# Optimization experiments

Hardware: AMD Instinct MI355X
Metric: run time of the kernel (lower is better)

## Reference

```python
import jax, jax.numpy as jnp
import numpy as np

D_MODEL = 1024
D_STATE = 16
D_CONV = 4
EXPAND = 2
MLP_EXPAND = 2
D_INNER = EXPAND * D_MODEL          # 2048
DT_RANK = (D_MODEL + 15) // 16      # 64
BATCH, SEQ = 2, 1024


def setup_inputs() -> dict:
    key = jax.random.key(0)
    ks = jax.random.split(key, 16)
    s = 0.02
    inp = {
        "x": jax.random.normal(ks[0], (BATCH, SEQ, D_MODEL), jnp.float32),
        "norm1_g": jnp.ones((D_MODEL,), jnp.float32),
        "norm1_b": jnp.zeros((D_MODEL,), jnp.float32),
        "in_proj_w": jax.random.normal(ks[1], (2 * D_INNER, D_MODEL), jnp.float32) * s,
        "conv_w": jax.random.normal(ks[2], (D_INNER, 1, D_CONV), jnp.float32) * s,
        "conv_b": jnp.zeros((D_INNER,), jnp.float32),
        "x_proj_w": jax.random.normal(ks[3], (DT_RANK + 2 * D_STATE, D_INNER), jnp.float32) * s,
        "dt_proj_w": jax.random.normal(ks[4], (D_INNER, DT_RANK), jnp.float32) * s,
        "dt_proj_b": jax.random.normal(ks[5], (D_INNER,), jnp.float32) * 0.1,
        "A_log": jnp.log(jnp.broadcast_to(jnp.arange(1, D_STATE + 1, dtype=jnp.float32), (D_INNER, D_STATE))),
        "D_param": jnp.ones((D_INNER,), jnp.float32),
        "out_proj_w": jax.random.normal(ks[6], (D_MODEL, D_INNER), jnp.float32) * s,
        "norm2_g": jnp.ones((D_MODEL,), jnp.float32),
        "norm2_b": jnp.zeros((D_MODEL,), jnp.float32),
        "mlp_w1": jax.random.normal(ks[7], (MLP_EXPAND * D_MODEL, D_MODEL), jnp.float32) * s,
        "mlp_b1": jnp.zeros((MLP_EXPAND * D_MODEL,), jnp.float32),
        "mlp_w2": jax.random.normal(ks[8], (D_MODEL, MLP_EXPAND * D_MODEL), jnp.float32) * s,
        "mlp_b2": jnp.zeros((D_MODEL,), jnp.float32),
    }
    return inp


def _layernorm(x, g, b, eps=1e-5):
    m = jnp.mean(x, axis=-1, keepdims=True)
    v = jnp.var(x, axis=-1, keepdims=True)
    return (x - m) * jax.lax.rsqrt(v + eps) * g + b


def _silu(x):
    return x * jax.nn.sigmoid(x)


def _mamba(x, in_proj_w, conv_w, conv_b, x_proj_w, dt_proj_w, dt_proj_b, A_log, D_param, out_proj_w):
    # x: (B, L, d_model)
    xz = x @ in_proj_w.T                              # (B, L, 2*Di)
    xc, z = jnp.split(xz, 2, axis=-1)                 # each (B, L, Di)
    # causal depthwise conv over time
    xc_t = xc.transpose(0, 2, 1)                      # (B, Di, L)
    xc_t = jax.lax.conv_general_dilated(
        xc_t, conv_w, window_strides=(1,), padding=[(D_CONV - 1, 0)],
        dimension_numbers=("NCH", "OIH", "NCH"), feature_group_count=D_INNER,
    ) + conv_b[None, :, None]
    xc = _silu(xc_t).transpose(0, 2, 1)               # (B, L, Di)

    dbc = xc @ x_proj_w.T                             # (B, L, dt_rank + 2N)
    dt, Bm, Cm = jnp.split(dbc, [DT_RANK, DT_RANK + D_STATE], axis=-1)
    dt = jax.nn.softplus(dt @ dt_proj_w.T + dt_proj_b)  # (B, L, Di)
    A = -jnp.exp(A_log)                               # (Di, N)

    def step(h, inp):
        dt_t, B_t, C_t, x_t = inp                     # (B,Di),(B,N),(B,N),(B,Di)
        dA = jnp.exp(dt_t[..., None] * A)             # (B, Di, N)
        h = dA * h + (dt_t * x_t)[..., None] * B_t[:, None, :]
        y = jnp.einsum("bdn,bn->bd", h, C_t)
        return h, y

    h0 = jnp.zeros((x.shape[0], D_INNER, D_STATE), x.dtype)
    xs = (dt.transpose(1, 0, 2), Bm.transpose(1, 0, 2), Cm.transpose(1, 0, 2), xc.transpose(1, 0, 2))
    _, ys = jax.lax.scan(step, h0, xs)                # ys: (L, B, Di)
    y = ys.transpose(1, 0, 2) + xc * D_param          # skip term D*x
    y = y * _silu(z)
    return y @ out_proj_w.T                           # (B, L, d_model)


def reference(x, norm1_g, norm1_b, in_proj_w, conv_w, conv_b, x_proj_w, dt_proj_w,
              dt_proj_b, A_log, D_param, out_proj_w, norm2_g, norm2_b,
              mlp_w1, mlp_b1, mlp_w2, mlp_b2):
    # residual + Mamba(LN(x))  (droppath=0 -> identity)
    h = x + _mamba(_layernorm(x, norm1_g, norm1_b), in_proj_w, conv_w, conv_b,
                   x_proj_w, dt_proj_w, dt_proj_b, A_log, D_param, out_proj_w)
    # residual + MLP(LN(h))    (dropout eval -> identity)
    m = _layernorm(h, norm2_g, norm2_b)
    m = jax.nn.gelu(m @ mlp_w1.T + mlp_b1, approximate=False) @ mlp_w2.T + mlp_b2
    return h + m
```

## Files before the change

kernel.cpp:

```cpp
#include <hip/hip_runtime.h>
#include <math.h>

#define D_MODEL 1024
#define D_INNER 2048
#define DT_RANK 64
#define D_STATE 16
#define NBC 96
#define BATCH 2
#define SEQ 1024
#define TOK (BATCH*SEQ)
#define CS 32
#define NCH 32
#define XKSPLIT 16

typedef __attribute__((ext_vector_type(8))) short short8;
typedef __attribute__((ext_vector_type(4))) float f32x4;
typedef __attribute__((ext_vector_type(4))) unsigned short us4;

__device__ __forceinline__ float softplus_f(float x) {
    return (x > 20.0f) ? x : log1pf(__expf(x));
}
__device__ __forceinline__ float gelu_f(float x) {
    return 0.5f * x * (1.0f + erff(x * 0.70710678118654752f));
}
__device__ __forceinline__ float silu_f(float x) {
    return x / (1.0f + __expf(-x));
}
__device__ __forceinline__ ushort f2bf(float f) {
    unsigned u = __float_as_uint(f);
    unsigned r = (u + 0x7fffu + ((u >> 16) & 1u)) >> 16;
    return (ushort)r;
}
__device__ __forceinline__ float bf2f(ushort u) {
    return __uint_as_float(((unsigned)u) << 16);
}

__global__ void convert_weights_kernel(const float* __restrict__ Wp, const float* __restrict__ Wo,
                                       const float* __restrict__ W1, const float* __restrict__ W2,
                                       const float* __restrict__ Wx, const float* __restrict__ Wdt,
                                       ushort* __restrict__ Wpb, ushort* __restrict__ Wob,
                                       ushort* __restrict__ W1b, ushort* __restrict__ W2b,
                                       ushort* __restrict__ Wxb, ushort* __restrict__ Wdtb) {
    int i = blockIdx.x * 256 + threadIdx.x;
    const float* src; ushort* dst; int off;
    if      (i < 1048576) { src = Wp;  dst = Wpb;  off = i; }
    else if (i < 1572864) { src = Wo;  dst = Wob;  off = i - 1048576; }
    else if (i < 2097152) { src = W1;  dst = W1b;  off = i - 1572864; }
    else if (i < 2621440) { src = W2;  dst = W2b;  off = i - 2097152; }
    else if (i < 2670592) { src = Wx;  dst = Wxb;  off = i - 2621440; }
    else if (i < 2703360) { src = Wdt; dst = Wdtb; off = i - 2670592; }
    else return;
    float4 v = ((const float4*)src)[off];
    ushort4 o;
    o.x = f2bf(v.x); o.y = f2bf(v.y); o.z = f2bf(v.z); o.w = f2bf(v.w);
    ((ushort4*)dst)[off] = o;
}

__global__ void ln_bf16_kernel(const float* __restrict__ x, const float* __restrict__ g,
                               const float* __restrict__ b, ushort* __restrict__ out) {
    int row = blockIdx.x;
    const float* xr = x + (size_t)row * D_MODEL;
    ushort* outr = out + (size_t)row * D_MODEL;
    int tid = threadIdx.x;
    float4 v = ((const float4*)xr)[tid];
    float s  = v.x + v.y + v.z + v.w;
    float sq = v.x*v.x + v.y*v.y + v.z*v.z + v.w*v.w;
    #pragma unroll
    for (int o = 32; o > 0; o >>= 1) {
        s  += __shfl_down(s,  o);
        sq += __shfl_down(sq, o);
    }
    __shared__ float ss[4], ssq[4];
    int wid = tid >> 6, lane = tid & 63;
    if (lane == 0) { ss[wid] = s; ssq[wid] = sq; }
    __syncthreads();
    if (tid == 0) {
        float a = 0.f, c = 0.f;
        for (int i = 0; i < 4; i++) { a += ss[i]; c += ssq[i]; }
        ss[0] = a; ssq[0] = c;
    }
    __syncthreads();
    float mean = ss[0] * (1.0f / D_MODEL);
    float var  = ssq[0] * (1.0f / D_MODEL) - mean * mean;
    float rstd = rsqrtf(var + 1e-5f);
    float4 gg = ((const float4*)g)[tid];
    float4 bb = ((const float4*)b)[tid];
    ushort4 o;
    o.x = f2bf((v.x - mean) * rstd * gg.x + bb.x);
    o.y = f2bf((v.y - mean) * rstd * gg.y + bb.y);
    o.z = f2bf((v.z - mean) * rstd * gg.z + bb.z);
    o.w = f2bf((v.w - mean) * rstd * gg.w + bb.w);
    ((ushort4*)outr)[tid] = o;
}

template<int BM, int BN, int ACT, bool BIAS, bool RES, bool OUTBF>
__global__ __launch_bounds__(256)
void mfma_gemm(const ushort* __restrict__ A, const ushort* __restrict__ W,
               const float* __restrict__ bias,
               const float* __restrict__ res, int ldr,
               void* __restrict__ Cout, int ldc, int K) {
    constexpr int WM = BM / 2, WN = BN / 2, FM = WM / 16, FN = WN / 16;
    __shared__ __align__(16) ushort As[BM * 32];
    __shared__ __align__(16) ushort Ws[BN * 32];
    const int tid  = threadIdx.x;
    const int lane = tid & 63, w = tid >> 6;
    const int wr = w >> 1, wc = w & 1;
    const int row0 = blockIdx.y * BM, col0 = blockIdx.x * BN;
    const int l16 = lane >> 4, l15 = lane & 15;
    const int srow = tid >> 2;
    const int scol = (tid & 3) * 8;

    f32x4 acc[FM][FN] = {};

    for (int k0 = 0; k0 < K; k0 += 32) {
        #pragma unroll
        for (int s = 0; s < BM / 64; s++) {
            const ushort* g = A + (size_t)(row0 + s * 64 + srow) * K + k0 + scol;
            __builtin_amdgcn_global_load_lds(
                (const __attribute__((address_space(1))) void*)g,
                (__attribute__((address_space(3))) void*)((char*)As + s * 4096 + w * 1024),
                16, 0, 0);
        }
        #pragma unroll
        for (int s = 0; s < BN / 64; s++) {
            const ushort* g = W + (size_t)(col0 + s * 64 + srow) * K + k0 + scol;
            __builtin_amdgcn_global_load_lds(
                (const __attribute__((address_space(1))) void*)g,
                (__attribute__((address_space(3))) void*)((char*)Ws + s * 4096 + w * 1024),
                16, 0, 0);
        }
        __syncthreads();

        short8 a[FM], b[FN];
        #pragma unroll
        for (int m = 0; m < FM; m++)
            a[m] = *(const short8*)(As + (wr * WM + m * 16 + l15) * 32 + l16 * 8);
        #pragma unroll
        for (int n = 0; n < FN; n++)
            b[n] = *(const short8*)(Ws + (wc * WN + n * 16 + l15) * 32 + l16 * 8);
        #pragma unroll
        for (int m = 0; m < FM; m++)
            #pragma unroll
            for (int n = 0; n < FN; n++)
                acc[m][n] = __builtin_amdgcn_mfma_f32_16x16x32_bf16(a[m], b[n], acc[m][n], 0, 0, 0);
        __syncthreads();
    }

    #pragma unroll
    for (int m = 0; m < FM; m++) {
        const int r0 = row0 + wr * WM + m * 16 + l16 * 4;
        #pragma unroll
        for (int n = 0; n < FN; n++) {
            const int c = col0 + wc * WN + n * 16 + l15;
            const float bv = BIAS ? bias[c] : 0.f;
            #pragma unroll
            for (int q = 0; q < 4; q++) {
                const int r = r0 + q;
                float v = acc[m][n][q] + bv;
                if (ACT == 1) v = softplus_f(v);
                else if (ACT == 2) v = gelu_f(v);
                if (RES) v += res[(size_t)r * ldr + c];
                if (OUTBF) ((ushort*)Cout)[(size_t)r * ldc + c] = f2bf(v);
                else       ((float*)Cout)[(size_t)r * ldc + c] = v;
            }
        }
    }
}

__global__ __launch_bounds__(256)
void xproj_split_kernel(const ushort* __restrict__ A,
                        const ushort* __restrict__ W,
                        float* __restrict__ part) {
    __shared__ __align__(16) ushort As[128 * 64];
    __shared__ __align__(16) ushort Bs[96 * 64];
    const int tid = threadIdx.x;
    const int lane = tid & 63, w = tid >> 6;
    const int l16 = lane >> 4, l15 = lane & 15;
    const int kbase = blockIdx.x * (D_INNER / XKSPLIT);
    const int row0 = blockIdx.y * 128;
    const int srow = tid >> 3;
    const int scol = (tid & 7) * 8;

    f32x4 acc[2][6] = {};

    for (int k0 = 0; k0 < D_INNER / XKSPLIT; k0 += 64) {
        #pragma unroll
        for (int s = 0; s < 4; s++) {
            const ushort* g = A + (size_t)(row0 + s * 32 + srow) * D_INNER + kbase + k0 + scol;
            __builtin_amdgcn_global_load_lds(
                (const __attribute__((address_space(1))) void*)g,
                (__attribute__((address_space(3))) void*)((char*)As + s * 4096 + w * 1024),
                16, 0, 0);
        }
        #pragma unroll
        for (int s = 0; s < 3; s++) {
            const ushort* g = W + (size_t)(s * 32 + srow) * D_INNER + kbase + k0 + scol;
            __builtin_amdgcn_global_load_lds(
                (const __attribute__((address_space(1))) void*)g,
                (__attribute__((address_space(3))) void*)((char*)Bs + s * 4096 + w * 1024),
                16, 0, 0);
        }
        __syncthreads();
        #pragma unroll
        for (int ks = 0; ks < 2; ks++) {
            short8 a[2], b[6];
            #pragma unroll
            for (int m = 0; m < 2; m++)
                a[m] = *(const short8*)(As + (w * 32 + m * 16 + l15) * 64 + ks * 32 + l16 * 8);
            #pragma unroll
            for (int n = 0; n < 6; n++)
                b[n] = *(const short8*)(Bs + (n * 16 + l15) * 64 + ks * 32 + l16 * 8);
            #pragma unroll
            for (int m = 0; m < 2; m++)
                #pragma unroll
                for (int n = 0; n < 6; n++)
                    acc[m][n] = __builtin_amdgcn_mfma_f32_16x16x32_bf16(a[m], b[n], acc[m][n], 0, 0, 0);
        }
        __syncthreads();
    }

    float* p = part + (size_t)blockIdx.x * D_INNER * NBC;
    #pragma unroll
    for (int m = 0; m < 2; m++) {
        const int r0 = row0 + w * 32 + m * 16 + l16 * 4;
        #pragma unroll
        for (int n = 0; n < 6; n++) {
            const int c = n * 16 + l15;
            #pragma unroll
            for (int q = 0; q < 4; q++)
                p[(size_t)(r0 + q) * NBC + c] = acc[m][n][q];
        }
    }
}

__global__ void xproj_reduce_kernel(const float* __restrict__ part,
                                    float* __restrict__ dbc, ushort* __restrict__ dtin_b) {
    int i = blockIdx.x * 256 + threadIdx.x;
    if (i >= D_INNER * NBC) return;
    float s = 0.f;
    #pragma unroll
    for (int k = 0; k < XKSPLIT; k++) s += part[(size_t)k * D_INNER * NBC + i];
    dbc[i] = s;
    int r = i / NBC, c = i - r * NBC;
    if (c < DT_RANK) dtin_b[r * DT_RANK + c] = f2bf(s);
}

__global__ void conv_silu_kernel(const ushort* __restrict__ xzb, const float* __restrict__ cw,
                                 const float* __restrict__ cb, ushort* __restrict__ xcb) {
    int idx = blockIdx.x * 256 + threadIdx.x;
    int c  = idx & (D_INNER - 1);
    int bt = idx >> 11;
    int b  = bt >> 10;
    int t  = bt & (SEQ - 1);
    float acc = cb[c];
    #pragma unroll
    for (int j = 0; j < 4; j++) {
        int tt = t - 3 + j;
        if (tt >= 0) acc += cw[c*4 + j] * bf2f(xzb[((size_t)(b*SEQ + tt)) * 4096 + c]);
    }
    xcb[idx] = f2bf(silu_f(acc));
}

__global__ __launch_bounds__(256)
void scan_chunk_kernel(const float* __restrict__ dtb, const float* __restrict__ dbc,
                       const ushort* __restrict__ xcb, const float* __restrict__ A_log,
                       float* __restrict__ chunkA, float* __restrict__ chunkH) {
    __shared__ float  dtS[64][36];
    __shared__ ushort xS[64][36];
    __shared__ float  BS[16][36];
    const int bid = blockIdx.x;
    const int dg = bid & 31, cc = (bid >> 5) & 31, b = bid >> 10;
    const int d0 = dg * 64;
    const int tid = threadIdx.x, lane = tid & 63, wv = tid >> 6;
    const int rbase = b * SEQ + cc * CS;

    #pragma unroll
    for (int k = 0; k < 8; k++) {
        int tt = k * 4 + wv;
        size_t row = (size_t)(rbase + tt);
        dtS[lane][tt] = dtb[row * D_INNER + d0 + lane];
        xS[lane][tt]  = xcb[row * D_INNER + d0 + lane];
    }
    #pragma unroll
    for (int k = 0; k < 2; k++) {
        int ii = k * 256 + tid;
        int val = ii & 15, tt = ii >> 4;
        BS[val][tt] = dbc[(size_t)(rbase + tt) * NBC + DT_RANK + val];
    }
    __syncthreads();

    const int d_local = tid >> 2, ng = tid & 3, nb = ng * 4;
    const int d = d0 + d_local;
    float Arow[4];
    #pragma unroll
    for (int j = 0; j < 4; j++) Arow[j] = -__expf(A_log[d * D_STATE + nb + j]);
    float h[4] = {};
    float ap[4] = {1.f, 1.f, 1.f, 1.f};
    #pragma unroll
    for (int it = 0; it < 8; ++it) {
        f32x4 dt4 = *(const f32x4*)&dtS[d_local][it * 4];
        us4   xu  = *(const us4*)&xS[d_local][it * 4];
        f32x4 Bv[4];
        #pragma unroll
        for (int j = 0; j < 4; j++) Bv[j] = *(const f32x4*)&BS[nb + j][it * 4];
        #pragma unroll
        for (int q = 0; q < 4; ++q) {
            float dtv = dt4[q];
            float dtx = dtv * bf2f(xu[q]);
            #pragma unroll
            for (int j = 0; j < 4; j++) {
                float dA = __expf(dtv * Arow[j]);
                ap[j] *= dA;
                h[j] = dA * h[j] + dtx * Bv[j][q];
            }
        }
    }
    size_t obase = ((size_t)((b * NCH + cc) * D_STATE) + nb) * D_INNER + d;
    #pragma unroll
    for (int j = 0; j < 4; j++) {
        chunkA[obase + (size_t)j * D_INNER] = ap[j];
        chunkH[obase + (size_t)j * D_INNER] = h[j];
    }
}

__global__ void scan_combine_kernel(const float* __restrict__ chunkA, float* __restrict__ chunkH) {
    int idx = blockIdx.x * 256 + threadIdx.x;
    int d = idx & (D_INNER - 1);
    int r = idx >> 11;
    int n = r & (D_STATE - 1);
    int b = r >> 4;
    float h = 0.f;
    for (int c = 0; c < NCH; c++) {
        size_t o = ((size_t)((b * NCH + c) * D_STATE + n)) * D_INNER + d;
        float a  = chunkA[o];
        float hl = chunkH[o];
        chunkH[o] = h;
        h = a * h + hl;
    }
}

__global__ __launch_bounds__(256)
void scan_final_kernel(const float* __restrict__ dtb, const float* __restrict__ dbc,
                       const ushort* __restrict__ xcb, const float* __restrict__ A_log,
                       const float* __restrict__ chunkH, const ushort* __restrict__ xzb,
                       const float* __restrict__ Dp, ushort* __restrict__ yb) {
    __shared__ float  dtS[64][36];
    __shared__ ushort xS[64][36];
    __shared__ ushort zS[64][36];
    __shared__ float  BS[16][36];
    __shared__ float  CSld[16][36];
    __shared__ ushort ySt[64][36];
    const int bid = blockIdx.x;
    const int dg = bid & 31, cc = (bid >> 5) & 31, b = bid >> 10;
    const int d0 = dg * 64;
    const int tid = threadIdx.x, lane = tid & 63, wv = tid >> 6;
    const int rbase = b * SEQ + cc * CS;

    #pragma unroll
    for (int k = 0; k < 8; k++) {
        int tt = k * 4 + wv;
        size_t row = (size_t)(rbase + tt);
        dtS[lane][tt] = dtb[row * D_INNER + d0 + lane];
        xS[lane][tt]  = xcb[row * D_INNER + d0 + lane];
        zS[lane][tt]  = xzb[row * 4096 + 2048 + d0 + lane];
    }
    #pragma unroll
    for (int k = 0; k < 4; k++) {
        int ii = k * 256 + tid;
        int val = ii & 31, tt = ii >> 5;
        float v = dbc[(size_t)(rbase + tt) * NBC + DT_RANK + val];
        if (val < 16) BS[val][tt] = v;
        else          CSld[val - 16][tt] = v;
    }
    __syncthreads();

    const int d_local = tid >> 2, ng = tid & 3, nb = ng * 4;
    const int d = d0 + d_local;
    float Arow[4];
    #pragma unroll
    for (int j = 0; j < 4; j++) Arow[j] = -__expf(A_log[d * D_STATE + nb + j]);
    float h[4];
    size_t obase = ((size_t)((b * NCH + cc) * D_STATE) + nb) * D_INNER + d;
    #pragma unroll
    for (int j = 0; j < 4; j++) h[j] = chunkH[obase + (size_t)j * D_INNER];
    const float Dpv = Dp[d];

    #pragma unroll
    for (int it = 0; it < 8; ++it) {
        f32x4 dt4 = *(const f32x4*)&dtS[d_local][it * 4];
        us4   xu  = *(const us4*)&xS[d_local][it * 4];
        f32x4 Bv[4], Cv[4];
        #pragma unroll
        for (int j = 0; j < 4; j++) {
            Bv[j] = *(const f32x4*)&BS[nb + j][it * 4];
            Cv[j] = *(const f32x4*)&CSld[nb + j][it * 4];
        }
        float yv4[4];
        #pragma unroll
        for (int q = 0; q < 4; ++q) {
            float dtv = dt4[q];
            float dtx = dtv * bf2f(xu[q]);
            float yv = 0.f;
            #pragma unroll
            for (int j = 0; j < 4; j++) {
                float dA = __expf(dtv * Arow[j]);
                h[j] = dA * h[j] + dtx * Bv[j][q];
                yv += h[j] * Cv[j][q];
            }
            yv4[q] = yv;
        }
        #pragma unroll
        for (int q = 0; q < 4; ++q) {
            yv4[q] += __shfl_xor(yv4[q], 1);
            yv4[q] += __shfl_xor(yv4[q], 2);
        }
        if (ng == 0) {
            us4 zu = *(const us4*)&zS[d_local][it * 4];
            us4 xo = *(const us4*)&xS[d_local][it * 4];
            us4 o;
            #pragma unroll
            for (int q = 0; q < 4; ++q) {
                float z = bf2f(zu[q]);
                o[q] = f2bf((yv4[q] + bf2f(xo[q]) * Dpv) * silu_f(z));
            }
            *(us4*)&ySt[d_local][it * 4] = o;
        }
    }
    __syncthreads();
    #pragma unroll
    for (int k = 0; k < 8; k++) {
        int tt = k * 4 + wv;
        yb[(size_t)(rbase + tt) * D_INNER + d0 + lane] = ySt[lane][tt];
    }
}

extern "C" void kernel_launch(void* const* d_in, const int* in_sizes, int n_in,
                              void* d_out, int out_size, void* d_ws, size_t ws_size,
                              hipStream_t stream) {
    const float* x    = (const float*)d_in[0];
    const float* n1g  = (const float*)d_in[1];
    const float* n1b  = (const float*)d_in[2];
    const float* Wp   = (const float*)d_in[3];
    const float* cw   = (const float*)d_in[4];
    const float* cb   = (const float*)d_in[5];
    const float* Wx   = (const float*)d_in[6];
    const float* Wdt  = (const float*)d_in[7];
    const float* bdt  = (const float*)d_in[8];
    const float* Alog = (const float*)d_in[9];
    const float* Dp   = (const float*)d_in[10];
    const float* Wo   = (const float*)d_in[11];
    const float* n2g  = (const float*)d_in[12];
    const float* n2b  = (const float*)d_in[13];
    const float* W1   = (const float*)d_in[14];
    const float* b1   = (const float*)d_in[15];
    const float* W2   = (const float*)d_in[16];
    const float* b2   = (const float*)d_in[17];
    float* out = (float*)d_out;
    float* ws  = (float*)d_ws;

    const size_t M1 = 1024 * 1024;
    ushort* xzb   = (ushort*)ws;
    ushort* xcb   = (ushort*)(ws + 8*M1);
    float*  dtb   = ws + 10*M1;
    float*  part  = ws + 14*M1;
    float*  hbuf  = ws + 14*M1;
    float*  dbc   = ws + 18*M1;
    ushort* dtin_b= (ushort*)(ws + 18*M1 + 262144);
    ushort* xnb   = (ushort*)(ws + 18*M1 + 524288);
    ushort* mb    = xnb;
    ushort* yb    = (ushort*)(ws + 20*M1);
    ushort* t1b   = yb;
    ushort* Wpb   = (ushort*)(ws + 22*M1);
    float*  chunkA= ws + 22*M1;
    ushort* Wob   = (ushort*)(ws + 24*M1);
    ushort* W1b   = (ushort*)(ws + 25*M1);
    ushort* W2b   = (ushort*)(ws + 26*M1);
    ushort* Wxb   = (ushort*)(ws + 27*M1);
    ushort* Wdtb  = (ushort*)(ws + 27*M1 + 131072);
    float*  chunkH = out;

    convert_weights_kernel<<<(2703360 + 255)/256, 256, 0, stream>>>(
        Wp, Wo, W1, W2, Wx, Wdt, Wpb, Wob, W1b, W2b, Wxb, Wdtb);

    ln_bf16_kernel<<<TOK, 256, 0, stream>>>(x, n1g, n1b, xnb);
    mfma_gemm<128,128,0,false,false,true><<<dim3(4096/128, 2048/128), 256, 0, stream>>>(
        xnb, Wpb, nullptr, nullptr, 0, xzb, 2*D_INNER, D_MODEL);
    conv_silu_kernel<<<TOK*D_INNER/256, 256, 0, stream>>>(xzb, cw, cb, xcb);
    xproj_split_kernel<<<dim3(XKSPLIT, 2048/128), 256, 0, stream>>>(xcb, Wxb, part);
    xproj_reduce_kernel<<<(D_INNER*NBC + 255)/256, 256, 0, stream>>>(part, dbc, dtin_b);
    mfma_gemm<128,128,1,true,false,false><<<dim3(2048/128, 2048/128), 256, 0, stream>>>(
        dtin_b, Wdtb, bdt, nullptr, 0, dtb, D_INNER, DT_RANK);
    scan_chunk_kernel<<<BATCH*NCH*(D_INNER/64), 256, 0, stream>>>(dtb, dbc, xcb, Alog, chunkA, chunkH);
    scan_combine_kernel<<<BATCH*D_STATE*D_INNER/256, 256, 0, stream>>>(chunkA, chunkH);
    scan_final_kernel<<<BATCH*NCH*(D_INNER/64), 256, 0, stream>>>(dtb, dbc, xcb, Alog, chunkH,
                                                                  xzb, Dp, yb);
    mfma_gemm<128,64,0,false,true,false><<<dim3(1024/64, 2048/128), 256, 0, stream>>>(
        yb, Wob, nullptr, x, D_MODEL, hbuf, D_MODEL, D_INNER);
    ln_bf16_kernel<<<TOK, 256, 0, stream>>>(hbuf, n2g, n2b, mb);
    mfma_gemm<128,128,2,true,false,true><<<dim3(2048/128, 2048/128), 256, 0, stream>>>(
        mb, W1b, b1, nullptr, 0, t1b, D_INNER, D_MODEL);
    mfma_gemm<128,64,0,true,true,false><<<dim3(1024/64, 2048/128), 256, 0, stream>>>(
        t1b, W2b, b2, hbuf, D_MODEL, out, D_MODEL, D_INNER);
}
```

Baseline: 267.3 us.

## Double-buffer LDS tiles in GEMM kernels and store dt as bf16

```diff
diff --git a/kernel.cpp b/kernel.cpp
--- a/kernel.cpp
+++ b/kernel.cpp
@@ -100,8 +100,8 @@
                const float* __restrict__ res, int ldr,
                void* __restrict__ Cout, int ldc, int K) {
     constexpr int WM = BM / 2, WN = BN / 2, FM = WM / 16, FN = WN / 16;
-    __shared__ __align__(16) ushort As[BM * 32];
-    __shared__ __align__(16) ushort Ws[BN * 32];
+    __shared__ __align__(16) ushort As[2][BM * 32];
+    __shared__ __align__(16) ushort Ws[2][BN * 32];
     const int tid  = threadIdx.x;
     const int lane = tid & 63, w = tid >> 6;
     const int wr = w >> 1, wc = w & 1;
@@ -109,16 +109,18 @@
     const int l16 = lane >> 4, l15 = lane & 15;
     const int srow = tid >> 2;
     const int scol = (tid & 3) * 8;
+    const int nk = K / 32;
 
     f32x4 acc[FM][FN] = {};
 
-    for (int k0 = 0; k0 < K; k0 += 32) {
+    auto stage = [&](int kk, int buf) {
+        const int k0 = kk * 32;
         #pragma unroll
         for (int s = 0; s < BM / 64; s++) {
             const ushort* g = A + (size_t)(row0 + s * 64 + srow) * K + k0 + scol;
             __builtin_amdgcn_global_load_lds(
                 (const __attribute__((address_space(1))) void*)g,
-                (__attribute__((address_space(3))) void*)((char*)As + s * 4096 + w * 1024),
+                (__attribute__((address_space(3))) void*)((char*)&As[buf][0] + s * 4096 + w * 1024),
                 16, 0, 0);
         }
         #pragma unroll
@@ -126,18 +128,25 @@
             const ushort* g = W + (size_t)(col0 + s * 64 + srow) * K + k0 + scol;
             __builtin_amdgcn_global_load_lds(
                 (const __attribute__((address_space(1))) void*)g,
-                (__attribute__((address_space(3))) void*)((char*)Ws + s * 4096 + w * 1024),
+                (__attribute__((address_space(3))) void*)((char*)&Ws[buf][0] + s * 4096 + w * 1024),
                 16, 0, 0);
         }
-        __syncthreads();
+    };
+
+    stage(0, 0);
+    __syncthreads();
+
+    for (int kk = 0; kk < nk; kk++) {
+        const int cur = kk & 1;
+        if (kk + 1 < nk) stage(kk + 1, cur ^ 1);
 
         short8 a[FM], b[FN];
         #pragma unroll
         for (int m = 0; m < FM; m++)
-            a[m] = *(const short8*)(As + (wr * WM + m * 16 + l15) * 32 + l16 * 8);
+            a[m] = *(const short8*)(&As[cur][0] + (wr * WM + m * 16 + l15) * 32 + l16 * 8);
         #pragma unroll
         for (int n = 0; n < FN; n++)
-            b[n] = *(const short8*)(Ws + (wc * WN + n * 16 + l15) * 32 + l16 * 8);
+            b[n] = *(const short8*)(&Ws[cur][0] + (wc * WN + n * 16 + l15) * 32 + l16 * 8);
         #pragma unroll
         for (int m = 0; m < FM; m++)
             #pragma unroll
@@ -171,8 +180,8 @@
 void xproj_split_kernel(const ushort* __restrict__ A,
                         const ushort* __restrict__ W,
                         float* __restrict__ part) {
-    __shared__ __align__(16) ushort As[128 * 64];
-    __shared__ __align__(16) ushort Bs[96 * 64];
+    __shared__ __align__(16) ushort As[2][128 * 64];
+    __shared__ __align__(16) ushort Bs[2][96 * 64];
     const int tid = threadIdx.x;
     const int lane = tid & 63, w = tid >> 6;
     const int l16 = lane >> 4, l15 = lane & 15;
@@ -183,13 +192,13 @@
 
     f32x4 acc[2][6] = {};
 
-    for (int k0 = 0; k0 < D_INNER / XKSPLIT; k0 += 64) {
+    auto stage = [&](int k0, int buf) {
         #pragma unroll
         for (int s = 0; s < 4; s++) {
             const ushort* g = A + (size_t)(row0 + s * 32 + srow) * D_INNER + kbase + k0 + scol;
             __builtin_amdgcn_global_load_lds(
                 (const __attribute__((address_space(1))) void*)g,
-                (__attribute__((address_space(3))) void*)((char*)As + s * 4096 + w * 1024),
+                (__attribute__((address_space(3))) void*)((char*)&As[buf][0] + s * 4096 + w * 1024),
                 16, 0, 0);
         }
         #pragma unroll
@@ -197,19 +206,27 @@
             const ushort* g = W + (size_t)(s * 32 + srow) * D_INNER + kbase + k0 + scol;
             __builtin_amdgcn_global_load_lds(
                 (const __attribute__((address_space(1))) void*)g,
-                (__attribute__((address_space(3))) void*)((char*)Bs + s * 4096 + w * 1024),
+                (__attribute__((address_space(3))) void*)((char*)&Bs[buf][0] + s * 4096 + w * 1024),
                 16, 0, 0);
         }
-        __syncthreads();
+    };
+
+    stage(0, 0);
+    __syncthreads();
+
+    const int nk = (D_INNER / XKSPLIT) / 64;
+    for (int kk = 0; kk < nk; kk++) {
+        const int cur = kk & 1;
+        if (kk + 1 < nk) stage((kk + 1) * 64, cur ^ 1);
         #pragma unroll
         for (int ks = 0; ks < 2; ks++) {
             short8 a[2], b[6];
             #pragma unroll
             for (int m = 0; m < 2; m++)
-                a[m] = *(const short8*)(As + (w * 32 + m * 16 + l15) * 64 + ks * 32 + l16 * 8);
+                a[m] = *(const short8*)(&As[cur][0] + (w * 32 + m * 16 + l15) * 64 + ks * 32 + l16 * 8);
             #pragma unroll
             for (int n = 0; n < 6; n++)
-                b[n] = *(const short8*)(Bs + (n * 16 + l15) * 64 + ks * 32 + l16 * 8);
+                b[n] = *(const short8*)(&Bs[cur][0] + (n * 16 + l15) * 64 + ks * 32 + l16 * 8);
             #pragma unroll
             for (int m = 0; m < 2; m++)
                 #pragma unroll
@@ -262,10 +279,10 @@
 }
 
 __global__ __launch_bounds__(256)
-void scan_chunk_kernel(const float* __restrict__ dtb, const float* __restrict__ dbc,
+void scan_chunk_kernel(const ushort* __restrict__ dtb, const float* __restrict__ dbc,
                        const ushort* __restrict__ xcb, const float* __restrict__ A_log,
                        float* __restrict__ chunkA, float* __restrict__ chunkH) {
-    __shared__ float  dtS[64][36];
+    __shared__ ushort dtS[64][36];
     __shared__ ushort xS[64][36];
     __shared__ float  BS[16][36];
     const int bid = blockIdx.x;
@@ -298,14 +315,14 @@
     float ap[4] = {1.f, 1.f, 1.f, 1.f};
     #pragma unroll
     for (int it = 0; it < 8; ++it) {
-        f32x4 dt4 = *(const f32x4*)&dtS[d_local][it * 4];
-        us4   xu  = *(const us4*)&xS[d_local][it * 4];
+        us4 dtu = *(const us4*)&dtS[d_local][it * 4];
+        us4 xu  = *(const us4*)&xS[d_local][it * 4];
         f32x4 Bv[4];
         #pragma unroll
         for (int j = 0; j < 4; j++) Bv[j] = *(const f32x4*)&BS[nb + j][it * 4];
         #pragma unroll
         for (int q = 0; q < 4; ++q) {
-            float dtv = dt4[q];
+            float dtv = bf2f(dtu[q]);
             float dtx = dtv * bf2f(xu[q]);
             #pragma unroll
             for (int j = 0; j < 4; j++) {
@@ -340,11 +357,11 @@
 }
 
 __global__ __launch_bounds__(256)
-void scan_final_kernel(const float* __restrict__ dtb, const float* __restrict__ dbc,
+void scan_final_kernel(const ushort* __restrict__ dtb, const float* __restrict__ dbc,
                        const ushort* __restrict__ xcb, const float* __restrict__ A_log,
                        const float* __restrict__ chunkH, const ushort* __restrict__ xzb,
                        const float* __restrict__ Dp, ushort* __restrict__ yb) {
-    __shared__ float  dtS[64][36];
+    __shared__ ushort dtS[64][36];
     __shared__ ushort xS[64][36];
     __shared__ ushort zS[64][36];
     __shared__ float  BS[16][36];
@@ -387,8 +404,8 @@
 
     #pragma unroll
     for (int it = 0; it < 8; ++it) {
-        f32x4 dt4 = *(const f32x4*)&dtS[d_local][it * 4];
-        us4   xu  = *(const us4*)&xS[d_local][it * 4];
+        us4 dtu = *(const us4*)&dtS[d_local][it * 4];
+        us4 xu  = *(const us4*)&xS[d_local][it * 4];
         f32x4 Bv[4], Cv[4];
         #pragma unroll
         for (int j = 0; j < 4; j++) {
@@ -398,7 +415,7 @@
         float yv4[4];
         #pragma unroll
         for (int q = 0; q < 4; ++q) {
-            float dtv = dt4[q];
+            float dtv = bf2f(dtu[q]);
             float dtx = dtv * bf2f(xu[q]);
             float yv = 0.f;
             #pragma unroll
@@ -461,7 +478,7 @@
     const size_t M1 = 1024 * 1024;
     ushort* xzb   = (ushort*)ws;
     ushort* xcb   = (ushort*)(ws + 8*M1);
-    float*  dtb   = ws + 10*M1;
+    ushort* dtb_b = (ushort*)(ws + 10*M1);
     float*  part  = ws + 14*M1;
     float*  hbuf  = ws + 14*M1;
     float*  dbc   = ws + 18*M1;
@@ -488,11 +505,11 @@
     conv_silu_kernel<<<TOK*D_INNER/256, 256, 0, stream>>>(xzb, cw, cb, xcb);
     xproj_split_kernel<<<dim3(XKSPLIT, 2048/128), 256, 0, stream>>>(xcb, Wxb, part);
     xproj_reduce_kernel<<<(D_INNER*NBC + 255)/256, 256, 0, stream>>>(part, dbc, dtin_b);
-    mfma_gemm<128,128,1,true,false,false><<<dim3(2048/128, 2048/128), 256, 0, stream>>>(
-        dtin_b, Wdtb, bdt, nullptr, 0, dtb, D_INNER, DT_RANK);
-    scan_chunk_kernel<<<BATCH*NCH*(D_INNER/64), 256, 0, stream>>>(dtb, dbc, xcb, Alog, chunkA, chunkH);
+    mfma_gemm<128,128,1,true,false,true><<<dim3(2048/128, 2048/128), 256, 0, stream>>>(
+        dtin_b, Wdtb, bdt, nullptr, 0, dtb_b, D_INNER, DT_RANK);
+    scan_chunk_kernel<<<BATCH*NCH*(D_INNER/64), 256, 0, stream>>>(dtb_b, dbc, xcb, Alog, chunkA, chunkH);
     scan_combine_kernel<<<BATCH*D_STATE*D_INNER/256, 256, 0, stream>>>(chunkA, chunkH);
-    scan_final_kernel<<<BATCH*NCH*(D_INNER/64), 256, 0, stream>>>(dtb, dbc, xcb, Alog, chunkH,
+    scan_final_kernel<<<BATCH*NCH*(D_INNER/64), 256, 0, stream>>>(dtb_b, dbc, xcb, Alog, chunkH,
                                                                   xzb, Dp, yb);
     mfma_gemm<128,64,0,false,true,false><<<dim3(1024/64, 2048/128), 256, 0, stream>>>(
         yb, Wob, nullptr, x, D_MODEL, hbuf, D_MODEL, D_INNER);
```

Measured after the change: 257.3 us. 3.7% less time.
